# Kernel optimization log

Hardware: AMD Instinct MI355X
Metric: run time of the kernel (lower is better)

Reference implementation:

```python
import jax, jax.numpy as jnp
import numpy as np

E = 1_600_000
NODE_D = 64
EDGE_D = 32
HIDDEN = 128
OUT_D = 32
IN_D = EDGE_D + 2 * NODE_D  # 160


def setup_inputs() -> dict:
    key = jax.random.key(0)
    ks = jax.random.split(key, 8)
    src = jax.random.normal(ks[0], (E, NODE_D), dtype=jnp.float32)
    dest = jax.random.normal(ks[1], (E, NODE_D), dtype=jnp.float32)
    edge_attr = jax.random.normal(ks[2], (E, EDGE_D), dtype=jnp.float32)
    u = jax.random.normal(ks[3], (16, 16), dtype=jnp.float32)
    batch = jax.random.randint(ks[4], (E,), 0, 16, dtype=jnp.int64)
    # MLP params: Linear(IN_D, HIDDEN) -> ReLU -> Linear(HIDDEN, OUT_D)
    w1 = jax.random.normal(ks[5], (IN_D, HIDDEN), dtype=jnp.float32) / np.sqrt(IN_D)
    b1 = jnp.zeros((HIDDEN,), dtype=jnp.float32)
    w2 = jax.random.normal(ks[6], (HIDDEN, OUT_D), dtype=jnp.float32) / np.sqrt(HIDDEN)
    b2 = jnp.zeros((OUT_D,), dtype=jnp.float32)
    return {"src": src, "dest": dest, "edge_attr": edge_attr, "u": u,
            "batch": batch, "w1": w1, "b1": b1, "w2": w2, "b2": b2}


def reference(src, dest, edge_attr, u, batch, w1, b1, w2, b2):
    # out = MLP(cat([src, dest, edge_attr], axis=1)); u, batch unused (MetaLayer API)
    x = jnp.concatenate([src, dest, edge_attr], axis=1)  # [E, IN_D]
    h = jax.nn.relu(x @ w1 + b1)                          # [E, HIDDEN]
    return h @ w2 + b2                                    # [E, OUT_D]
```

## Files before the change

### kernel.cpp

```cpp
#include <hip/hip_runtime.h>


typedef float  f32x4  __attribute__((ext_vector_type(4)));
typedef short  s16x8  __attribute__((ext_vector_type(8)));
typedef unsigned short u16x4 __attribute__((ext_vector_type(4)));

#define SRC_STRIDE 144
#define EDG_STRIDE 80
#define WS_BYTES   (32 * SRC_STRIDE + 16 * EDG_STRIDE)

__device__ __forceinline__ unsigned short f2bf(float f) {
    unsigned int u = __float_as_uint(f);
    u += 0x7FFFu + ((u >> 16) & 1u);
    return (unsigned short)(u >> 16);
}

__global__ __launch_bounds__(1024, 1) void edge_mlp(
    const float* __restrict__ src, const float* __restrict__ dst,
    const float* __restrict__ edg, const float* __restrict__ w1,
    const float* __restrict__ b1, const float* __restrict__ w2,
    const float* __restrict__ b2, float* __restrict__ out, int ntiles)
{
    __shared__ __align__(16) unsigned short w1s[40 * 64 * 8];
    __shared__ __align__(16) float b1s[128];
    __shared__ __align__(16) unsigned short w2s[8 * 64 * 8];
    __shared__ __align__(16) float b2s[2 * 64 * 4];
    __shared__ __align__(16) char xs[16][WS_BYTES];

    const int t    = threadIdx.x;
    const int lane = t & 63;
    const int wid  = t >> 6;
    const int rq   = lane >> 4;
    const int rr   = lane & 15;

    for (int s = t; s < 40 * 64; s += 1024) {
        const int f  = s >> 6, l = s & 63;
        const int kk = f >> 3, n = f & 7;
        const int k0 = kk * 32 + ((l >> 4) << 3);
        const int cl = (n << 4) + (l & 15);
        union { s16x8 v; unsigned short u[8]; } r;
#pragma unroll
        for (int j = 0; j < 8; ++j)
            r.u[j] = f2bf(w1[(k0 + j) * 128 + cl]);
        *reinterpret_cast<s16x8*>(&w1s[s * 8]) = r.v;
    }
    if (t < 128) b1s[t] = b1[t];

    if (wid == 0) {
#pragma unroll
        for (int m = 0; m < 4; ++m)
#pragma unroll
            for (int n2 = 0; n2 < 2; ++n2) {
                union { s16x8 v; unsigned short u[8]; } r;
#pragma unroll
                for (int j = 0; j < 4; ++j) {
                    r.u[j]     = f2bf(w2[(m * 16 + rq * 4 + j) * 32 + n2 * 16 + rr]);
                    r.u[4 + j] = f2bf(w2[((m + 4) * 16 + rq * 4 + j) * 32 + n2 * 16 + rr]);
                }
                *reinterpret_cast<s16x8*>(&w2s[((m * 2 + n2) * 64 + lane) * 8]) = r.v;
            }
        *reinterpret_cast<f32x4*>(&b2s[(0 * 64 + lane) * 4]) =
            *reinterpret_cast<const f32x4*>(b2 + rq * 4);
        *reinterpret_cast<f32x4*>(&b2s[(1 * 64 + lane) * 4]) =
            *reinterpret_cast<const f32x4*>(b2 + 16 + rq * 4);
    }

    __syncthreads();

    char* const wsS = xs[wid];
    char* const wsD = xs[wid] + 16 * SRC_STRIDE;
    char* const wsE = xs[wid] + 32 * SRC_STRIDE;

    const int srow  = lane >> 4;
    const int scol8 = (lane & 15) * 8;
    const int erow  = lane >> 3;
    const int ecol8 = (lane & 7) * 8;

    for (int tile = blockIdx.x; tile < ntiles; tile += gridDim.x) {
        const size_t row0 = (size_t)tile * 256 + (size_t)wid * 16;

        const float* gs = src + row0 * 64 + lane * 4;
        const float* gd = dst + row0 * 64 + lane * 4;
        const float* ge = edg + row0 * 32 + lane * 4;
        f32x4 s0v, s1v, s2v, s3v, d0v, d1v, d2v, d3v, e0v, e1v;
        asm volatile(
            "global_load_dwordx4 %[s0], %[ps], off\n\t"
            "global_load_dwordx4 %[s1], %[ps], off offset:1024\n\t"
            "global_load_dwordx4 %[s2], %[ps], off offset:2048\n\t"
            "global_load_dwordx4 %[s3], %[ps], off offset:3072\n\t"
            "global_load_dwordx4 %[d0], %[pd], off\n\t"
            "global_load_dwordx4 %[d1], %[pd], off offset:1024\n\t"
            "global_load_dwordx4 %[d2], %[pd], off offset:2048\n\t"
            "global_load_dwordx4 %[d3], %[pd], off offset:3072\n\t"
            "global_load_dwordx4 %[e0], %[pe], off\n\t"
            "global_load_dwordx4 %[e1], %[pe], off offset:1024\n\t"
            "s_waitcnt vmcnt(0)"
            : [s0]"=&v"(s0v), [s1]"=&v"(s1v), [s2]"=&v"(s2v), [s3]"=&v"(s3v),
              [d0]"=&v"(d0v), [d1]"=&v"(d1v), [d2]"=&v"(d2v), [d3]"=&v"(d3v),
              [e0]"=&v"(e0v), [e1]"=&v"(e1v)
            : [ps]"v"(gs), [pd]"v"(gd), [pe]"v"(ge));

        {
            const f32x4 ls[4] = {s0v, s1v, s2v, s3v};
#pragma unroll
            for (int i = 0; i < 4; ++i) {
                u16x4 p = {f2bf(ls[i].x), f2bf(ls[i].y), f2bf(ls[i].z), f2bf(ls[i].w)};
                *reinterpret_cast<u16x4*>(wsS + (i * 4 + srow) * SRC_STRIDE + scol8) = p;
            }
            const f32x4 ld[4] = {d0v, d1v, d2v, d3v};
#pragma unroll
            for (int i = 0; i < 4; ++i) {
                u16x4 p = {f2bf(ld[i].x), f2bf(ld[i].y), f2bf(ld[i].z), f2bf(ld[i].w)};
                *reinterpret_cast<u16x4*>(wsD + (i * 4 + srow) * SRC_STRIDE + scol8) = p;
            }
            const f32x4 le[2] = {e0v, e1v};
#pragma unroll
            for (int i = 0; i < 2; ++i) {
                u16x4 p = {f2bf(le[i].x), f2bf(le[i].y), f2bf(le[i].z), f2bf(le[i].w)};
                *reinterpret_cast<u16x4*>(wsE + (i * 8 + erow) * EDG_STRIDE + ecol8) = p;
            }
        }

        f32x4 acc[8];
#pragma unroll
        for (int n = 0; n < 8; ++n)
            acc[n] = *reinterpret_cast<const f32x4*>(&b1s[n * 16 + rq * 4]);

#pragma unroll
        for (int kk = 0; kk < 5; ++kk) {
            const char* xb; int koff, strd;
            if      (kk == 0) { xb = wsS; koff = 0;  strd = SRC_STRIDE; }
            else if (kk == 1) { xb = wsS; koff = 64; strd = SRC_STRIDE; }
            else if (kk == 2) { xb = wsD; koff = 0;  strd = SRC_STRIDE; }
            else if (kk == 3) { xb = wsD; koff = 64; strd = SRC_STRIDE; }
            else              { xb = wsE; koff = 0;  strd = EDG_STRIDE; }
            s16x8 a = *reinterpret_cast<const s16x8*>(xb + rr * strd + koff + rq * 16);

#pragma unroll
            for (int n = 0; n < 8; ++n) {
                s16x8 wv = *reinterpret_cast<const s16x8*>(&w1s[((kk * 8 + n) * 64 + lane) * 8]);
                acc[n] = __builtin_amdgcn_mfma_f32_16x16x32_bf16(wv, a, acc[n], 0, 0, 0);
            }
        }

        f32x4 acc2[2];
        acc2[0] = *reinterpret_cast<const f32x4*>(&b2s[(0 * 64 + lane) * 4]);
        acc2[1] = *reinterpret_cast<const f32x4*>(&b2s[(1 * 64 + lane) * 4]);

#pragma unroll
        for (int m = 0; m < 4; ++m) {
            union { s16x8 v; unsigned short u[8]; } hh;
#pragma unroll
            for (int j = 0; j < 4; ++j) {
                hh.u[j]     = f2bf(fmaxf(acc[m][j], 0.0f));
                hh.u[4 + j] = f2bf(fmaxf(acc[m + 4][j], 0.0f));
            }
            s16x8 w20 = *reinterpret_cast<const s16x8*>(&w2s[((m * 2 + 0) * 64 + lane) * 8]);
            s16x8 w21 = *reinterpret_cast<const s16x8*>(&w2s[((m * 2 + 1) * 64 + lane) * 8]);
            acc2[0] = __builtin_amdgcn_mfma_f32_16x16x32_bf16(w20, hh.v, acc2[0], 0, 0, 0);
            acc2[1] = __builtin_amdgcn_mfma_f32_16x16x32_bf16(w21, hh.v, acc2[1], 0, 0, 0);
        }

        float* po = out + (row0 + rr) * 32;
        *reinterpret_cast<f32x4*>(po + rq * 4)      = acc2[0];
        *reinterpret_cast<f32x4*>(po + 16 + rq * 4) = acc2[1];
    }
}

__global__ void edge_mlp_tail(
    const float* __restrict__ src, const float* __restrict__ dst,
    const float* __restrict__ edg, const float* __restrict__ w1,
    const float* __restrict__ b1, const float* __restrict__ w2,
    const float* __restrict__ b2, float* __restrict__ out,
    long long row0, long long E)
{
    const long long r = row0 + blockIdx.x;
    if (r >= E) return;
    __shared__ float h[128];
    const int t = threadIdx.x;
    float acc = b1[t];
    for (int k = 0; k < 64; ++k) acc += src[r * 64 + k] * w1[k * 128 + t];
    for (int k = 0; k < 64; ++k) acc += dst[r * 64 + k] * w1[(64 + k) * 128 + t];
    for (int k = 0; k < 32; ++k) acc += edg[r * 32 + k] * w1[(128 + k) * 128 + t];
    h[t] = acc > 0.0f ? acc : 0.0f;
    __syncthreads();
    if (t < 32) {
        float o = b2[t];
        for (int k = 0; k < 128; ++k) o += h[k] * w2[k * 32 + t];
        out[r * 32 + t] = o;
    }
}

extern "C" void kernel_launch(void* const* d_in, const int* in_sizes, int n_in,
                              void* d_out, int out_size, void* d_ws, size_t ws_size,
                              hipStream_t stream)
{
    const float* src = (const float*)d_in[0];
    const float* dst = (const float*)d_in[1];
    const float* edg = (const float*)d_in[2];
    const float* w1  = (const float*)d_in[5];
    const float* b1  = (const float*)d_in[6];
    const float* w2  = (const float*)d_in[7];
    const float* b2  = (const float*)d_in[8];
    float* out = (float*)d_out;

    const long long E      = (long long)in_sizes[0] / 64;
    const int       ntiles = (int)(E / 256);
    const long long rem    = E - (long long)ntiles * 256;

    if (ntiles > 0) {
        int grid = ntiles < 256 ? ntiles : 256;
        edge_mlp<<<dim3(grid), dim3(1024), 0, stream>>>(
            src, dst, edg, w1, b1, w2, b2, out, ntiles);
    }
    if (rem > 0) {
        edge_mlp_tail<<<dim3((unsigned)rem), dim3(128), 0, stream>>>(
            src, dst, edg, w1, b1, w2, b2, out, (long long)ntiles * 256, E);
    }
}
```

Baseline: 255.3 us.

## Process two 16-row fragments per wave with overlapped loads and shared weight reads

Each wave now handles 32 rows per tile instead of 16. It issues global loads for both 16-row halves up front, then converts and stages the first half while the second half is still in flight, using a partial vmcnt wait. The first-layer MFMA loop reuses each w1 LDS fragment for both halves, halving weight LDS reads per row. This doubles the accumulator register footprint and halves the tile count, which may reduce load balance across the 256 blocks.

```diff
diff --git a/kernel.cpp b/kernel.cpp
--- a/kernel.cpp
+++ b/kernel.cpp
@@ -77,12 +77,17 @@
     const int ecol8 = (lane & 7) * 8;
 
     for (int tile = blockIdx.x; tile < ntiles; tile += gridDim.x) {
-        const size_t row0 = (size_t)tile * 256 + (size_t)wid * 16;
-
-        const float* gs = src + row0 * 64 + lane * 4;
-        const float* gd = dst + row0 * 64 + lane * 4;
-        const float* ge = edg + row0 * 32 + lane * 4;
-        f32x4 s0v, s1v, s2v, s3v, d0v, d1v, d2v, d3v, e0v, e1v;
+        const size_t row0 = (size_t)tile * 512 + (size_t)wid * 32;
+
+        const float* gsA = src + row0 * 64 + lane * 4;
+        const float* gdA = dst + row0 * 64 + lane * 4;
+        const float* geA = edg + row0 * 32 + lane * 4;
+        const float* gsB = gsA + 16 * 64;
+        const float* gdB = gdA + 16 * 64;
+        const float* geB = geA + 16 * 32;
+
+        f32x4 sA0, sA1, sA2, sA3, dA0, dA1, dA2, dA3, eA0, eA1;
+        f32x4 sB0, sB1, sB2, sB3, dB0, dB1, dB2, dB3, eB0, eB1;
         asm volatile(
             "global_load_dwordx4 %[s0], %[ps], off\n\t"
             "global_load_dwordx4 %[s1], %[ps], off offset:1024\n\t"
@@ -93,39 +98,53 @@
             "global_load_dwordx4 %[d2], %[pd], off offset:2048\n\t"
             "global_load_dwordx4 %[d3], %[pd], off offset:3072\n\t"
             "global_load_dwordx4 %[e0], %[pe], off\n\t"
-            "global_load_dwordx4 %[e1], %[pe], off offset:1024\n\t"
-            "s_waitcnt vmcnt(0)"
-            : [s0]"=&v"(s0v), [s1]"=&v"(s1v), [s2]"=&v"(s2v), [s3]"=&v"(s3v),
-              [d0]"=&v"(d0v), [d1]"=&v"(d1v), [d2]"=&v"(d2v), [d3]"=&v"(d3v),
-              [e0]"=&v"(e0v), [e1]"=&v"(e1v)
-            : [ps]"v"(gs), [pd]"v"(gd), [pe]"v"(ge));
+            "global_load_dwordx4 %[e1], %[pe], off offset:1024"
+            : [s0]"=&v"(sA0), [s1]"=&v"(sA1), [s2]"=&v"(sA2), [s3]"=&v"(sA3),
+              [d0]"=&v"(dA0), [d1]"=&v"(dA1), [d2]"=&v"(dA2), [d3]"=&v"(dA3),
+              [e0]"=&v"(eA0), [e1]"=&v"(eA1)
+            : [ps]"v"(gsA), [pd]"v"(gdA), [pe]"v"(geA));
+        asm volatile(
+            "global_load_dwordx4 %[s0], %[ps], off\n\t"
+            "global_load_dwordx4 %[s1], %[ps], off offset:1024\n\t"
+            "global_load_dwordx4 %[s2], %[ps], off offset:2048\n\t"
+            "global_load_dwordx4 %[s3], %[ps], off offset:3072\n\t"
+            "global_load_dwordx4 %[d0], %[pd], off\n\t"
+            "global_load_dwordx4 %[d1], %[pd], off offset:1024\n\t"
+            "global_load_dwordx4 %[d2], %[pd], off offset:2048\n\t"
+            "global_load_dwordx4 %[d3], %[pd], off offset:3072\n\t"
+            "global_load_dwordx4 %[e0], %[pe], off\n\t"
+            "global_load_dwordx4 %[e1], %[pe], off offset:1024"
+            : [s0]"=&v"(sB0), [s1]"=&v"(sB1), [s2]"=&v"(sB2), [s3]"=&v"(sB3),
+              [d0]"=&v"(dB0), [d1]"=&v"(dB1), [d2]"=&v"(dB2), [d3]"=&v"(dB3),
+              [e0]"=&v"(eB0), [e1]"=&v"(eB1)
+            : [ps]"v"(gsB), [pd]"v"(gdB), [pe]"v"(geB));
+
+        asm volatile("s_waitcnt vmcnt(10)"
+            : [s0]"+v"(sA0), [s1]"+v"(sA1), [s2]"+v"(sA2), [s3]"+v"(sA3),
+              [d0]"+v"(dA0), [d1]"+v"(dA1), [d2]"+v"(dA2), [d3]"+v"(dA3),
+              [e0]"+v"(eA0), [e1]"+v"(eA1));
 
         {
-            const f32x4 ls[4] = {s0v, s1v, s2v, s3v};
+            const f32x4 ls[4] = {sA0, sA1, sA2, sA3};
 #pragma unroll
             for (int i = 0; i < 4; ++i) {
                 u16x4 p = {f2bf(ls[i].x), f2bf(ls[i].y), f2bf(ls[i].z), f2bf(ls[i].w)};
                 *reinterpret_cast<u16x4*>(wsS + (i * 4 + srow) * SRC_STRIDE + scol8) = p;
             }
-            const f32x4 ld[4] = {d0v, d1v, d2v, d3v};
+            const f32x4 ld[4] = {dA0, dA1, dA2, dA3};
 #pragma unroll
             for (int i = 0; i < 4; ++i) {
                 u16x4 p = {f2bf(ld[i].x), f2bf(ld[i].y), f2bf(ld[i].z), f2bf(ld[i].w)};
                 *reinterpret_cast<u16x4*>(wsD + (i * 4 + srow) * SRC_STRIDE + scol8) = p;
             }
-            const f32x4 le[2] = {e0v, e1v};
+            const f32x4 le[2] = {eA0, eA1};
 #pragma unroll
             for (int i = 0; i < 2; ++i) {
                 u16x4 p = {f2bf(le[i].x), f2bf(le[i].y), f2bf(le[i].z), f2bf(le[i].w)};
                 *reinterpret_cast<u16x4*>(wsE + (i * 8 + erow) * EDG_STRIDE + ecol8) = p;
             }
         }
-
-        f32x4 acc[8];
-#pragma unroll
-        for (int n = 0; n < 8; ++n)
-            acc[n] = *reinterpret_cast<const f32x4*>(&b1s[n * 16 + rq * 4]);
-
+        s16x8 a0f[5], a1f[5];
 #pragma unroll
         for (int kk = 0; kk < 5; ++kk) {
             const char* xb; int koff, strd;
@@ -134,36 +153,84 @@
             else if (kk == 2) { xb = wsD; koff = 0;  strd = SRC_STRIDE; }
             else if (kk == 3) { xb = wsD; koff = 64; strd = SRC_STRIDE; }
             else              { xb = wsE; koff = 0;  strd = EDG_STRIDE; }
-            s16x8 a = *reinterpret_cast<const s16x8*>(xb + rr * strd + koff + rq * 16);
-
+            a0f[kk] = *reinterpret_cast<const s16x8*>(xb + rr * strd + koff + rq * 16);
+        }
+
+        asm volatile("s_waitcnt vmcnt(0)"
+            : [s0]"+v"(sB0), [s1]"+v"(sB1), [s2]"+v"(sB2), [s3]"+v"(sB3),
+              [d0]"+v"(dB0), [d1]"+v"(dB1), [d2]"+v"(dB2), [d3]"+v"(dB3),
+              [e0]"+v"(eB0), [e1]"+v"(eB1));
+        {
+            const f32x4 ls[4] = {sB0, sB1, sB2, sB3};
+#pragma unroll
+            for (int i = 0; i < 4; ++i) {
+                u16x4 p = {f2bf(ls[i].x), f2bf(ls[i].y), f2bf(ls[i].z), f2bf(ls[i].w)};
+                *reinterpret_cast<u16x4*>(wsS + (i * 4 + srow) * SRC_STRIDE + scol8) = p;
+            }
+            const f32x4 ld[4] = {dB0, dB1, dB2, dB3};
+#pragma unroll
+            for (int i = 0; i < 4; ++i) {
+                u16x4 p = {f2bf(ld[i].x), f2bf(ld[i].y), f2bf(ld[i].z), f2bf(ld[i].w)};
+                *reinterpret_cast<u16x4*>(wsD + (i * 4 + srow) * SRC_STRIDE + scol8) = p;
+            }
+            const f32x4 le[2] = {eB0, eB1};
+#pragma unroll
+            for (int i = 0; i < 2; ++i) {
+                u16x4 p = {f2bf(le[i].x), f2bf(le[i].y), f2bf(le[i].z), f2bf(le[i].w)};
+                *reinterpret_cast<u16x4*>(wsE + (i * 8 + erow) * EDG_STRIDE + ecol8) = p;
+            }
+        }
+#pragma unroll
+        for (int kk = 0; kk < 5; ++kk) {
+            const char* xb; int koff, strd;
+            if      (kk == 0) { xb = wsS; koff = 0;  strd = SRC_STRIDE; }
+            else if (kk == 1) { xb = wsS; koff = 64; strd = SRC_STRIDE; }
+            else if (kk == 2) { xb = wsD; koff = 0;  strd = SRC_STRIDE; }
+            else if (kk == 3) { xb = wsD; koff = 64; strd = SRC_STRIDE; }
+            else              { xb = wsE; koff = 0;  strd = EDG_STRIDE; }
+            a1f[kk] = *reinterpret_cast<const s16x8*>(xb + rr * strd + koff + rq * 16);
+        }
+
+        f32x4 acc0[8], acc1[8];
+#pragma unroll
+        for (int n = 0; n < 8; ++n) {
+            f32x4 b = *reinterpret_cast<const f32x4*>(&b1s[n * 16 + rq * 4]);
+            acc0[n] = b;
+            acc1[n] = b;
+        }
+#pragma unroll
+        for (int kk = 0; kk < 5; ++kk)
 #pragma unroll
             for (int n = 0; n < 8; ++n) {
                 s16x8 wv = *reinterpret_cast<const s16x8*>(&w1s[((kk * 8 + n) * 64 + lane) * 8]);
-                acc[n] = __builtin_amdgcn_mfma_f32_16x16x32_bf16(wv, a, acc[n], 0, 0, 0);
-            }
-        }
-
-        f32x4 acc2[2];
-        acc2[0] = *reinterpret_cast<const f32x4*>(&b2s[(0 * 64 + lane) * 4]);
-        acc2[1] = *reinterpret_cast<const f32x4*>(&b2s[(1 * 64 + lane) * 4]);
-
-#pragma unroll
-        for (int m = 0; m < 4; ++m) {
-            union { s16x8 v; unsigned short u[8]; } hh;
-#pragma unroll
-            for (int j = 0; j < 4; ++j) {
-                hh.u[j]     = f2bf(fmaxf(acc[m][j], 0.0f));
-                hh.u[4 + j] = f2bf(fmaxf(acc[m + 4][j], 0.0f));
-            }
-            s16x8 w20 = *reinterpret_cast<const s16x8*>(&w2s[((m * 2 + 0) * 64 + lane) * 8]);
-            s16x8 w21 = *reinterpret_cast<const s16x8*>(&w2s[((m * 2 + 1) * 64 + lane) * 8]);
-            acc2[0] = __builtin_amdgcn_mfma_f32_16x16x32_bf16(w20, hh.v, acc2[0], 0, 0, 0);
-            acc2[1] = __builtin_amdgcn_mfma_f32_16x16x32_bf16(w21, hh.v, acc2[1], 0, 0, 0);
-        }
-
-        float* po = out + (row0 + rr) * 32;
-        *reinterpret_cast<f32x4*>(po + rq * 4)      = acc2[0];
-        *reinterpret_cast<f32x4*>(po + 16 + rq * 4) = acc2[1];
+                acc0[n] = __builtin_amdgcn_mfma_f32_16x16x32_bf16(wv, a0f[kk], acc0[n], 0, 0, 0);
+                acc1[n] = __builtin_amdgcn_mfma_f32_16x16x32_bf16(wv, a1f[kk], acc1[n], 0, 0, 0);
+            }
+
+#pragma unroll
+        for (int rf = 0; rf < 2; ++rf) {
+            f32x4 acc2[2];
+            acc2[0] = *reinterpret_cast<const f32x4*>(&b2s[(0 * 64 + lane) * 4]);
+            acc2[1] = *reinterpret_cast<const f32x4*>(&b2s[(1 * 64 + lane) * 4]);
+
+#pragma unroll
+            for (int m = 0; m < 4; ++m) {
+                union { s16x8 v; unsigned short u[8]; } hh;
+#pragma unroll
+                for (int j = 0; j < 4; ++j) {
+                    hh.u[j]     = f2bf(fmaxf((rf == 0 ? acc0[m][j]     : acc1[m][j]),     0.0f));
+                    hh.u[4 + j] = f2bf(fmaxf((rf == 0 ? acc0[m + 4][j] : acc1[m + 4][j]), 0.0f));
+                }
+                s16x8 w20 = *reinterpret_cast<const s16x8*>(&w2s[((m * 2 + 0) * 64 + lane) * 8]);
+                s16x8 w21 = *reinterpret_cast<const s16x8*>(&w2s[((m * 2 + 1) * 64 + lane) * 8]);
+                acc2[0] = __builtin_amdgcn_mfma_f32_16x16x32_bf16(w20, hh.v, acc2[0], 0, 0, 0);
+                acc2[1] = __builtin_amdgcn_mfma_f32_16x16x32_bf16(w21, hh.v, acc2[1], 0, 0, 0);
+            }
+
+            float* po = out + (row0 + rf * 16 + rr) * 32;
+            *reinterpret_cast<f32x4*>(po + rq * 4)      = acc2[0];
+            *reinterpret_cast<f32x4*>(po + 16 + rq * 4) = acc2[1];
+        }
     }
 }
 
@@ -205,8 +272,8 @@
     float* out = (float*)d_out;
 
     const long long E      = (long long)in_sizes[0] / 64;
-    const int       ntiles = (int)(E / 256);
-    const long long rem    = E - (long long)ntiles * 256;
+    const int       ntiles = (int)(E / 512);
+    const long long rem    = E - (long long)ntiles * 512;
 
     if (ntiles > 0) {
         int grid = ntiles < 256 ? ntiles : 256;
@@ -215,6 +282,6 @@
     }
     if (rem > 0) {
         edge_mlp_tail<<<dim3((unsigned)rem), dim3(128), 0, stream>>>(
-            src, dst, edg, w1, b1, w2, b2, out, (long long)ntiles * 256, E);
-    }
-}
+            src, dst, edg, w1, b1, w2, b2, out, (long long)ntiles * 512, E);
+    }
+}
```

Result: slower. 342.8 us (+34.3%).
